# Optimization experiments

Measured on AMD Instinct MI355X. Metric: run time of the kernel, lower is better.

## Reference

```python
import jax, jax.numpy as jnp
import numpy as np

N, E = 50000, 300000
IN_DIM, CODE_DIM = 1024, 768
HID, HEADS, DH = 256, 4, 64
NUM_REL = 5
CODE_WEIGHT = 1.0


def setup_inputs() -> dict:
    key = jax.random.key(0)
    ks = jax.random.split(key, 24)
    p = lambda k, shape: jax.random.normal(k, shape, dtype=jnp.float32) * 0.05
    return {
        "x": jax.random.normal(ks[0], (N, IN_DIM), dtype=jnp.float32),
        "edge_index": jax.random.randint(ks[1], (2, E), 0, N, dtype=jnp.int64),
        "edge_type": jax.random.randint(ks[2], (E,), 0, NUM_REL, dtype=jnp.int64),
        "edge_weight": jax.random.uniform(ks[3], (E,), dtype=jnp.float32),
        "rel_emb": p(ks[4], (NUM_REL, HID)),
        "W_in": p(ks[5], (HID, IN_DIM)),
        "b_in": jnp.zeros((HID,), jnp.float32),
        "W1": p(ks[6], (HEADS * DH, HID)),
        "a1_src": p(ks[7], (HEADS, DH)),
        "a1_dst": p(ks[8], (HEADS, DH)),
        "b1": jnp.zeros((HEADS * DH,), jnp.float32),
        "W2": p(ks[9], (HEADS * DH, HID)),
        "a2_src": p(ks[10], (HEADS, DH)),
        "a2_dst": p(ks[11], (HEADS, DH)),
        "b2": jnp.zeros((HEADS * DH,), jnp.float32),
        "ln1_g": jnp.ones((HID,), jnp.float32),
        "ln1_b": jnp.zeros((HID,), jnp.float32),
        "ln2_g": jnp.ones((HID,), jnp.float32),
        "ln2_b": jnp.zeros((HID,), jnp.float32),
        "W_out": p(ks[12], (1, HID)),
        "b_out": jnp.zeros((1,), jnp.float32),
    }


def _layer_norm(x, g, b, eps=1e-5):
    m = x.mean(-1, keepdims=True)
    v = ((x - m) ** 2).mean(-1, keepdims=True)
    return (x - m) * jax.lax.rsqrt(v + eps) * g + b


def _gat_conv(h, s_all, d_all, W, a_src, a_dst, bias):
    # PyG GATConv (concat=True, negative_slope=0.2), self-loops already in s_all/d_all
    xh = (h @ W.T).reshape(N, HEADS, DH)                      # [N,H,DH]
    al_s = (xh * a_src).sum(-1)                                # [N,H]
    al_d = (xh * a_dst).sum(-1)                                # [N,H]
    e = jax.nn.leaky_relu(al_s[s_all] + al_d[d_all], 0.2)      # [E+N,H]
    mx = jax.ops.segment_max(e, d_all, num_segments=N)         # segment softmax over dst
    ex = jnp.exp(e - mx[d_all])
    den = jax.ops.segment_sum(ex, d_all, num_segments=N)
    alpha = ex / (den[d_all] + 1e-16)
    out = jax.ops.segment_sum(xh[s_all] * alpha[:, :, None], d_all, num_segments=N)
    return out.reshape(N, HEADS * DH) + bias


def reference(x, edge_index, edge_type, edge_weight, rel_emb, W_in, b_in,
              W1, a1_src, a1_dst, b1, W2, a2_src, a2_dst, b2,
              ln1_g, ln1_b, ln2_g, ln2_b, W_out, b_out):
    # split (code_at_front=True), standardize numeric, l2-normalize code
    x_code = x[:, :CODE_DIM]
    x_num = x[:, CODE_DIM:]
    m = x_num.mean(0, keepdims=True)
    s = jnp.maximum(x_num.std(0, ddof=1, keepdims=True), 1e-6)
    x_num = (x_num - m) / s
    nrm = jnp.maximum(jnp.linalg.norm(x_code, axis=1, keepdims=True), 1e-12)
    x_code = x_code / nrm
    xin = jnp.concatenate([x_num, CODE_WEIGHT * x_code], axis=-1)

    h = jax.nn.relu(xin @ W_in.T + b_in)                       # [N,HID]

    src, dst = edge_index[0], edge_index[1]
    rel = rel_emb[edge_type] * edge_weight[:, None]            # [E,HID]
    msg = h[src] + rel
    h = h.at[dst].add(msg)                                     # index_add

    loop = jnp.arange(N, dtype=src.dtype)                      # GATConv add_self_loops
    s_all = jnp.concatenate([src, loop])
    d_all = jnp.concatenate([dst, loop])

    h1 = _gat_conv(h, s_all, d_all, W1, a1_src, a1_dst, b1)
    h = _layer_norm(h1 + h, ln1_g, ln1_b)
    h2 = _gat_conv(h, s_all, d_all, W2, a2_src, a2_dst, b2)
    h = _layer_norm(h2 + h, ln2_g, ln2_b)
    return (h @ W_out.T + b_out).squeeze(-1)                   # [N]
```

## Files before the change

kernel.cpp:

```cpp
#include <hip/hip_runtime.h>
#include <math.h>

constexpr int NN   = 50000;
constexpr int EE   = 300000;
constexpr int IND  = 1024;
constexpr int CODE = 768;
constexpr int HID  = 256;

typedef __bf16 bf16_t;
typedef bf16_t bf16x4 __attribute__((ext_vector_type(4)));
typedef bf16_t bf16x8 __attribute__((ext_vector_type(8)));
typedef float  f32x4  __attribute__((ext_vector_type(4)));

__device__ __forceinline__ f32x4 mfma16(bf16x8 a, bf16x8 b, f32x4 c) {
    return __builtin_amdgcn_mfma_f32_16x16x32_bf16(a, b, c, 0, 0, 0);
}

#define GLOAD_LDS16(gp, lp) __builtin_amdgcn_global_load_lds(                         \
    (__attribute__((address_space(1))) void*)(gp),                                    \
    (__attribute__((address_space(3))) void*)(lp), 16, 0, 0)

__device__ __forceinline__ void cvt_split(f32x4 u0, f32x4 u1, bf16x8& hi, bf16x8& lo) {
    #pragma unroll
    for (int i = 0; i < 4; i++) {
        bf16_t h0 = (bf16_t)u0[i];
        hi[i]     = h0;
        lo[i]     = (bf16_t)(u0[i] - (float)h0);
        bf16_t h1 = (bf16_t)u1[i];
        hi[4 + i] = h1;
        lo[4 + i] = (bf16_t)(u1[i] - (float)h1);
    }
}

__device__ __forceinline__ bf16x8 cvt_hi(f32x4 u0, f32x4 u1) {
    bf16x8 h;
    #pragma unroll
    for (int i = 0; i < 4; i++) {
        h[i]     = (bf16_t)u0[i];
        h[4 + i] = (bf16_t)u1[i];
    }
    return h;
}

__device__ __forceinline__ f32x4 ld_bf4(const bf16_t* p) {
    bf16x4 v = *(const bf16x4*)p;
    f32x4 r;
    r[0] = (float)v[0]; r[1] = (float)v[1]; r[2] = (float)v[2]; r[3] = (float)v[3];
    return r;
}

__global__ void colstats_kernel(const float* __restrict__ x, float* __restrict__ sums) {
    int col = threadIdx.x;
    float s = 0.f, s2 = 0.f;
    for (int row = blockIdx.x; row < NN; row += gridDim.x) {
        float v = x[(size_t)row * IND + CODE + col];
        s += v; s2 += v * v;
    }
    atomicAdd(&sums[col], s);
    atomicAdd(&sums[256 + col], s2);
}

__global__ void rownorm_kernel(const float* __restrict__ x, float* __restrict__ invnorm) {
    int lane = threadIdx.x & 63;
    int wid  = threadIdx.x >> 6;
    int row  = blockIdx.x * 4 + wid;
    if (row >= NN) return;
    const float4* x4 = (const float4*)(x + (size_t)row * IND);
    float s = 0.f;
    #pragma unroll
    for (int i = 0; i < 3; i++) {
        float4 v = x4[lane + i * 64];
        s += v.x * v.x + v.y * v.y + v.z * v.z + v.w * v.w;
    }
    #pragma unroll
    for (int off = 32; off; off >>= 1) s += __shfl_xor(s, off);
    if (lane == 0) invnorm[row] = 1.f / fmaxf(sqrtf(s), 1e-12f);
}

__global__ void prep_w_kernel(const float* __restrict__ W, const float* __restrict__ sums,
                              const float* __restrict__ b_in, bf16_t* __restrict__ Wh,
                              float* __restrict__ cb)
{
    int c = blockIdx.x, t = threadIdx.x;
    float mean = sums[t] / (float)NN;
    float var  = (sums[256 + t] - (float)NN * mean * mean) / (float)(NN - 1);
    float sd   = fmaxf(sqrtf(fmaxf(var, 0.f)), 1e-6f);
    float invstd = 1.f / sd;

    const float* wr = W + (size_t)c * IND;
    bf16_t* wh = Wh + (size_t)c * IND;
    for (int k = t; k < 768; k += 256) wh[k] = (bf16_t)wr[256 + k];
    wh[768 + t] = (bf16_t)(wr[t] * invstd);

    float p = wr[t] * invstd * mean;
    #pragma unroll
    for (int off = 32; off; off >>= 1) p += __shfl_xor(p, off);
    __shared__ float ps[4];
    if ((t & 63) == 0) ps[t >> 6] = p;
    __syncthreads();
    if (t == 0) cb[c] = b_in[c] - (ps[0] + ps[1] + ps[2] + ps[3]);
}

__global__ void prep_ws_kernel(const float* __restrict__ W1, const float* __restrict__ W2,
                               bf16_t* __restrict__ Wh1, bf16_t* __restrict__ Wh2)
{
    int c = blockIdx.x, t = threadIdx.x;
    if (c < 256) Wh1[(size_t)c * 256 + t] = (bf16_t)W1[(size_t)c * 256 + t];
    else {
        int cc = c - 256;
        Wh2[(size_t)cc * 256 + t] = (bf16_t)W2[(size_t)cc * 256 + t];
    }
}


__device__ __forceinline__ void stage_a(const float* __restrict__ src, int ldk,
                                        int rowbase, int maxrow, int k0,
                                        float* ldsbuf, int tid) {
    int w = tid >> 6, l = tid & 63;
    int lr = l >> 3, lc = l & 7;
    int g  = lc ^ lr;
    #pragma unroll
    for (int i = 0; i < 4; i++) {
        int rloc = i * 32 + w * 8;
        float* dst = ldsbuf + rloc * 32;
        int row = rowbase + rloc + lr;
        if (row > maxrow) row = maxrow;
        const float* gp = src + (size_t)row * ldk + k0 + g * 4;
        GLOAD_LDS16(gp, dst);
    }
}

__device__ __forceinline__ void stage_b(const bf16_t* __restrict__ src, int n0, int ldk,
                                        int k0, bf16_t* buf, int tid) {
    int w = tid >> 6, l = tid & 63;
    #pragma unroll
    for (int i = 0; i < 2; i++) {
        int gbase = w * 128 + i * 64;
        bf16_t* dst = buf + gbase * 8;
        int g = gbase + l;
        int col = g >> 2, p = g & 3;
        int gs = p ^ ((col >> 1) & 3);
        const bf16_t* gp = src + (size_t)(n0 + col) * ldk + k0 + gs * 8;
        GLOAD_LDS16(gp, dst);
    }
}

template<int MODE, int K, int FATTN>
__global__ __launch_bounds__(256) void gemm_mfma_kernel(
    const float* __restrict__ A, const bf16_t* __restrict__ Bh,
    const float* __restrict__ cb, const float* __restrict__ invnorm,
    const float* __restrict__ a_src, const float* __restrict__ a_dst,
    float* __restrict__ out, bf16_t* __restrict__ xhb,
    float* __restrict__ al_s, float* __restrict__ al_d)
{
    __shared__ float  As[2][128 * 32];
    __shared__ bf16_t Bhs[2][128 * 32];
    __shared__ float inv_s[128];
    constexpr int NT = K / 32;

    int tid  = threadIdx.x;
    int lane = tid & 63;
    int w    = tid >> 6;
    int wr   = w >> 1, wc = w & 1;
    int r0   = blockIdx.x * 128, n0 = blockIdx.y * 128;

    if (MODE == 1 && tid < 128) {
        int r = r0 + tid;
        inv_s[tid] = (r < NN) ? invnorm[r] : 1.f;
    }

    f32x4 acc[4][4];
    #pragma unroll
    for (int i = 0; i < 4; i++)
        #pragma unroll
        for (int j = 0; j < 4; j++) acc[i][j] = (f32x4)0.f;

    int kc = lane >> 4, fr = lane & 15;

    stage_a(A, K, r0, NN - 1, 0, As[0], tid);
    stage_b(Bh, n0, K, 0, Bhs[0], tid);
    __syncthreads();

    for (int t = 0; t < NT; ++t) {
        int buf = t & 1;
        if (t + 1 < NT) {
            stage_a(A, K, r0, NN - 1, (t + 1) * 32, As[buf ^ 1], tid);
            stage_b(Bh, n0, K, (t + 1) * 32, Bhs[buf ^ 1], tid);
        }
        if (MODE == 1 && t == 24) {
            #pragma unroll
            for (int mf = 0; mf < 4; mf++) {
                f32x4 iv = *(const f32x4*)&inv_s[wr * 64 + mf * 16 + kc * 4];
                #pragma unroll
                for (int nf = 0; nf < 4; nf++)
                    #pragma unroll
                    for (int j = 0; j < 4; j++) acc[mf][nf][j] *= iv[j];
            }
        }
        const float*  Ab = As[buf];
        const bf16_t* Hb = Bhs[buf];
        bf16x8 ahi[4], alo[4];
        #pragma unroll
        for (int mf = 0; mf < 4; mf++) {
            int r  = wr * 64 + mf * 16 + fr;
            int rb = r * 32, r7 = r & 7;
            f32x4 u0 = *(const f32x4*)&Ab[rb + (((2 * kc + 0) ^ r7) << 2)];
            f32x4 u1 = *(const f32x4*)&Ab[rb + (((2 * kc + 1) ^ r7) << 2)];
            if (MODE == 1) cvt_split(u0, u1, ahi[mf], alo[mf]);
            else           ahi[mf] = cvt_hi(u0, u1);
        }
        #pragma unroll
        for (int nf = 0; nf < 4; nf++) {
            int c  = wc * 64 + nf * 16 + fr;
            int pr = kc ^ ((c >> 1) & 3);
            bf16x8 bhi = *(const bf16x8*)&Hb[c * 32 + pr * 8];
            #pragma unroll
            for (int mf = 0; mf < 4; mf++) {
                acc[mf][nf] = mfma16(ahi[mf], bhi, acc[mf][nf]);
                if (MODE == 1) acc[mf][nf] = mfma16(alo[mf], bhi, acc[mf][nf]);
            }
        }
        __syncthreads();
    }

    int head = blockIdx.y * 2 + wc;
    float asv[4], adv[4];
    if (FATTN) {
        #pragma unroll
        for (int nf = 0; nf < 4; nf++) {
            asv[nf] = a_src[head * 64 + nf * 16 + fr];
            adv[nf] = a_dst[head * 64 + nf * 16 + fr];
        }
    }
    #pragma unroll
    for (int mf = 0; mf < 4; mf++) {
        #pragma unroll
        for (int j = 0; j < 4; j++) {
            int row = r0 + wr * 64 + mf * 16 + kc * 4 + j;
            bool ok = row < NN;
            float s = 0.f, d = 0.f;
            #pragma unroll
            for (int nf = 0; nf < 4; nf++) {
                int col = n0 + wc * 64 + nf * 16 + fr;
                float v = acc[mf][nf][j];
                if (MODE == 1) {
                    v = fmaxf(v + cb[col], 0.f);
                    if (ok) out[(size_t)row * HID + col] = v;
                }
                if (FATTN) {
                    s += v * asv[nf]; d += v * adv[nf];
                    if (ok) xhb[(size_t)row * HID + col] = (bf16_t)v;
                }
            }
            if (FATTN) {
                #pragma unroll
                for (int off = 1; off < 16; off <<= 1) {
                    s += __shfl_xor(s, off);
                    d += __shfl_xor(d, off);
                }
                if (ok && fr == 0) {
                    al_s[row * 4 + head] = s;
                    al_d[row * 4 + head] = d;
                }
            }
        }
    }
}

__global__ void deg_kernel(const int* __restrict__ ei, int* __restrict__ deg) {
    int e = blockIdx.x * 256 + threadIdx.x;
    if (e < EE) atomicAdd(&deg[ei[EE + e]], 1);
}

constexpr int SCB = 1024;
constexpr int SCN = (NN + SCB - 1) / SCB;

__global__ void scan_pass1(const int* __restrict__ deg, int* __restrict__ bsum) {
    int b = blockIdx.x, t = threadIdx.x;
    int base = b * SCB + t * 4;
    int s = 0;
    #pragma unroll
    for (int i = 0; i < 4; i++) { int idx = base + i; if (idx < NN) s += deg[idx]; }
    #pragma unroll
    for (int off = 32; off; off >>= 1) s += __shfl_xor(s, off);
    __shared__ int ps[4];
    if ((t & 63) == 0) ps[t >> 6] = s;
    __syncthreads();
    if (t == 0) bsum[b] = ps[0] + ps[1] + ps[2] + ps[3];
}

__global__ void scan_pass2(int* __restrict__ bsum) {
    int t = threadIdx.x;
    int orig = (t < SCN) ? bsum[t] : 0;
    int v = orig;
    for (int off = 1; off < 64; off <<= 1) {
        int u = __shfl_up(v, off);
        if (t >= off) v += u;
    }
    if (t < SCN) bsum[t] = v - orig;
}

__global__ void scan_pass3(const int* __restrict__ deg, const int* __restrict__ boffs,
                           int* __restrict__ row_ptr, int* __restrict__ cursor) {
    int b = blockIdx.x, t = threadIdx.x;
    int base = b * SCB + t * 4;
    int d[4]; int tot = 0;
    #pragma unroll
    for (int i = 0; i < 4; i++) { int idx = base + i; d[i] = (idx < NN) ? deg[idx] : 0; tot += d[i]; }
    int v = tot;
    for (int off = 1; off < 64; off <<= 1) {
        int u = __shfl_up(v, off);
        if ((t & 63) >= off) v += u;
    }
    __shared__ int wsum[4];
    if ((t & 63) == 63) wsum[t >> 6] = v;
    __syncthreads();
    int woff = 0;
    for (int j = 0; j < (t >> 6); j++) woff += wsum[j];
    int run = boffs[b] + woff + v - tot;
    #pragma unroll
    for (int i = 0; i < 4; i++) {
        int idx = base + i;
        if (idx < NN) {
            cursor[idx] = run;
            run += d[i];
            row_ptr[idx + 1] = run;
        }
    }
    if (b == 0 && t == 0) row_ptr[0] = 0;
}

__global__ void fill_kernel(const int* __restrict__ ei, const int* __restrict__ etype,
                            const float* __restrict__ ew, int* __restrict__ cursor,
                            int* __restrict__ csr_src, int* __restrict__ csr_t,
                            float* __restrict__ csr_w) {
    int e = blockIdx.x * 256 + threadIdx.x;
    if (e >= EE) return;
    int dst = ei[EE + e];
    int pos = atomicAdd(&cursor[dst], 1);
    csr_src[pos] = ei[e];
    csr_t[pos]   = etype[e];
    csr_w[pos]   = ew[e];
}

__global__ void relagg_kernel(const float* __restrict__ h, const int* __restrict__ row_ptr,
                              const int* __restrict__ csr_src, const int* __restrict__ csr_t,
                              const float* __restrict__ csr_w,
                              const float* __restrict__ rel_emb, float* __restrict__ out)
{
    int lane = threadIdx.x & 63, wid = threadIdx.x >> 6;
    int node = blockIdx.x * 4 + wid;
    if (node >= NN) return;
    int c0 = lane * 4;
    f32x4 acc = *(const f32x4*)(h + (size_t)node * HID + c0);
    float wsum[5] = {0.f, 0.f, 0.f, 0.f, 0.f};
    int beg = row_ptr[node], end = row_ptr[node + 1];
    int k = beg;
    for (; k + 4 <= end; k += 4) {
        int s[4], tt[4]; float ww[4];
        #pragma unroll
        for (int j = 0; j < 4; j++) {
            s[j]  = csr_src[k + j];
            tt[j] = csr_t[k + j];
            ww[j] = csr_w[k + j];
        }
        f32x4 xv[4];
        #pragma unroll
        for (int j = 0; j < 4; j++) xv[j] = *(const f32x4*)(h + (size_t)s[j] * HID + c0);
        #pragma unroll
        for (int j = 0; j < 4; j++) {
            acc += xv[j];
            #pragma unroll
            for (int r = 0; r < 5; r++) wsum[r] += (tt[j] == r) ? ww[j] : 0.f;
        }
    }
    for (; k < end; k++) {
        int src = csr_src[k]; int t = csr_t[k]; float w = csr_w[k];
        acc += *(const f32x4*)(h + (size_t)src * HID + c0);
        #pragma unroll
        for (int r = 0; r < 5; r++) wsum[r] += (t == r) ? w : 0.f;
    }
    #pragma unroll
    for (int r = 0; r < 5; r++)
        acc += wsum[r] * *(const f32x4*)(rel_emb + r * HID + c0);
    *(f32x4*)(out + (size_t)node * HID + c0) = acc;
}

template<int FINAL>
__global__ void gat_kernel(const bf16_t* __restrict__ xhb, const float* __restrict__ al_s,
                           const float* __restrict__ al_d, const int* __restrict__ row_ptr,
                           const int* __restrict__ csr_src, const float* __restrict__ h_res,
                           const float* __restrict__ bias, const float* __restrict__ ln_g,
                           const float* __restrict__ ln_b, float* __restrict__ out,
                           const float* __restrict__ W_out, const float* __restrict__ b_out,
                           float* __restrict__ final_out)
{
    int lane = threadIdx.x & 63, wid = threadIdx.x >> 6;
    int node = blockIdx.x * 4 + wid;
    if (node >= NN) return;
    int hh = lane >> 4;
    int c0 = lane * 4;

    float ald = al_d[node * 4 + hh];
    float m, den;
    f32x4 acc;

    {
        float als = al_s[node * 4 + hh];
        float e = als + ald;
        e = (e >= 0.f) ? e : 0.2f * e;
        m = e; den = 1.f;
        acc = ld_bf4(xhb + (size_t)node * HID + c0);
    }

    int beg = row_ptr[node], end = row_ptr[node + 1];
    int k = beg;
    for (; k + 4 <= end; k += 4) {
        int s[4];
        #pragma unroll
        for (int j = 0; j < 4; j++) s[j] = csr_src[k + j];
        float als[4];
        #pragma unroll
        for (int j = 0; j < 4; j++) als[j] = al_s[s[j] * 4 + hh];
        f32x4 xv[4];
        #pragma unroll
        for (int j = 0; j < 4; j++) xv[j] = ld_bf4(xhb + (size_t)s[j] * HID + c0);
        #pragma unroll
        for (int j = 0; j < 4; j++) {
            float e = als[j] + ald;
            e = (e >= 0.f) ? e : 0.2f * e;
            float mn  = fmaxf(m, e);
            float f   = __expf(m - mn);
            float wgt = __expf(e - mn);
            m   = mn;
            den = den * f + wgt;
            acc = acc * f + wgt * xv[j];
        }
    }
    for (; k < end; k++) {
        int src = csr_src[k];
        float als = al_s[src * 4 + hh];
        f32x4 xv = ld_bf4(xhb + (size_t)src * HID + c0);
        float e = als + ald;
        e = (e >= 0.f) ? e : 0.2f * e;
        float mn  = fmaxf(m, e);
        float f   = __expf(m - mn);
        float wgt = __expf(e - mn);
        m   = mn;
        den = den * f + wgt;
        acc = acc * f + wgt * xv;
    }

    f32x4 bia = *(const f32x4*)(bias + c0);
    f32x4 res = *(const f32x4*)(h_res + (size_t)node * HID + c0);
    f32x4 z;
    float rd = 1.f / (den + 1e-16f);
    #pragma unroll
    for (int i = 0; i < 4; i++) z[i] = acc[i] * rd + bia[i] + res[i];

    float s = z[0] + z[1] + z[2] + z[3];
    #pragma unroll
    for (int off = 32; off; off >>= 1) s += __shfl_xor(s, off);
    float mean = s * (1.f / 256.f);
    float vp = 0.f;
    #pragma unroll
    for (int i = 0; i < 4; i++) { float d2 = z[i] - mean; vp += d2 * d2; }
    #pragma unroll
    for (int off = 32; off; off >>= 1) vp += __shfl_xor(vp, off);
    float rstd = rsqrtf(vp * (1.f / 256.f) + 1e-5f);

    f32x4 g = *(const f32x4*)(ln_g + c0);
    f32x4 bb = *(const f32x4*)(ln_b + c0);
    if (FINAL) {
        f32x4 wo = *(const f32x4*)(W_out + c0);
        float dot = 0.f;
        #pragma unroll
        for (int i = 0; i < 4; i++)
            dot += ((z[i] - mean) * rstd * g[i] + bb[i]) * wo[i];
        #pragma unroll
        for (int off = 32; off; off >>= 1) dot += __shfl_xor(dot, off);
        if (lane == 0) final_out[node] = dot + b_out[0];
    } else {
        f32x4 o;
        #pragma unroll
        for (int i = 0; i < 4; i++) o[i] = (z[i] - mean) * rstd * g[i] + bb[i];
        *(f32x4*)(out + (size_t)node * HID + c0) = o;
    }
}

extern "C" void kernel_launch(void* const* d_in, const int* in_sizes, int n_in,
                              void* d_out, int out_size, void* d_ws, size_t ws_size,
                              hipStream_t stream) {
    const float* x       = (const float*)d_in[0];
    const int*   ei      = (const int*)d_in[1];
    const int*   etype   = (const int*)d_in[2];
    const float* ew      = (const float*)d_in[3];
    const float* rel_emb = (const float*)d_in[4];
    const float* W_in    = (const float*)d_in[5];
    const float* b_in    = (const float*)d_in[6];
    const float* W1      = (const float*)d_in[7];
    const float* a1s     = (const float*)d_in[8];
    const float* a1d     = (const float*)d_in[9];
    const float* b1      = (const float*)d_in[10];
    const float* W2      = (const float*)d_in[11];
    const float* a2s     = (const float*)d_in[12];
    const float* a2d     = (const float*)d_in[13];
    const float* b2      = (const float*)d_in[14];
    const float* ln1g    = (const float*)d_in[15];
    const float* ln1b    = (const float*)d_in[16];
    const float* ln2g    = (const float*)d_in[17];
    const float* ln2b    = (const float*)d_in[18];
    const float* W_out   = (const float*)d_in[19];
    const float* b_out   = (const float*)d_in[20];
    float* out = (float*)d_out;

    char* ws = (char*)d_ws;
    auto alloc = [&](size_t bytes) {
        void* p = (void*)ws;
        ws += (bytes + 255) & ~(size_t)255;
        return p;
    };
    float*  bufA     = (float*)alloc((size_t)NN * HID * 4);
    float*  bufB     = (float*)alloc((size_t)NN * HID * 4);
    bf16_t* xhb      = (bf16_t*)alloc((size_t)NN * HID * 2);
    bf16_t* wmh      = (bf16_t*)alloc((size_t)HID * IND * 2);
    bf16_t* w1h      = (bf16_t*)alloc((size_t)HID * HID * 2);
    bf16_t* w2h      = (bf16_t*)alloc((size_t)HID * HID * 2);
    float*  cbv      = (float*)alloc(256 * 4);
    float*  stats_s  = (float*)alloc(512 * 4);
    float*  invnorm  = (float*)alloc((size_t)NN * 4);
    float*  al_s     = (float*)alloc((size_t)NN * 4 * 4);
    float*  al_d     = (float*)alloc((size_t)NN * 4 * 4);
    int*    deg      = (int*)alloc((size_t)NN * 4);
    int*    row_ptr  = (int*)alloc((size_t)(NN + 1) * 4);
    int*    cursor   = (int*)alloc((size_t)NN * 4);
    int*    csr_src  = (int*)alloc((size_t)EE * 4);
    int*    csr_t    = (int*)alloc((size_t)EE * 4);
    float*  csr_w    = (float*)alloc((size_t)EE * 4);
    int*    bsum     = (int*)alloc(64 * 4);

    hipMemsetAsync(stats_s, 0, 512 * 4, stream);
    hipMemsetAsync(deg, 0, (size_t)NN * 4, stream);

    colstats_kernel<<<1024, 256, 0, stream>>>(x, stats_s);
    rownorm_kernel<<<(NN + 3) / 4, 256, 0, stream>>>(x, invnorm);
    prep_w_kernel<<<256, 256, 0, stream>>>(W_in, stats_s, b_in, wmh, cbv);
    prep_ws_kernel<<<512, 256, 0, stream>>>(W1, W2, w1h, w2h);

    deg_kernel<<<(EE + 255) / 256, 256, 0, stream>>>(ei, deg);
    scan_pass1<<<SCN, 256, 0, stream>>>(deg, bsum);
    scan_pass2<<<1, 64, 0, stream>>>(bsum);
    scan_pass3<<<SCN, 256, 0, stream>>>(deg, bsum, row_ptr, cursor);
    fill_kernel<<<(EE + 255) / 256, 256, 0, stream>>>(ei, etype, ew, cursor,
                                                      csr_src, csr_t, csr_w);

    dim3 g1((NN + 127) / 128, 2);

    gemm_mfma_kernel<1, 1024, 0><<<g1, 256, 0, stream>>>(
        x, wmh, cbv, invnorm, nullptr, nullptr, bufA, nullptr, nullptr, nullptr);

    int nodeBlocks = (NN + 3) / 4;

    relagg_kernel<<<nodeBlocks, 256, 0, stream>>>(bufA, row_ptr, csr_src, csr_t, csr_w,
                                                  rel_emb, bufB);

    gemm_mfma_kernel<0, 256, 1><<<g1, 256, 0, stream>>>(
        bufB, w1h, nullptr, nullptr, a1s, a1d, nullptr, xhb, al_s, al_d);
    gat_kernel<0><<<nodeBlocks, 256, 0, stream>>>(xhb, al_s, al_d, row_ptr, csr_src,
                                                  bufB, b1, ln1g, ln1b, bufA,
                                                  nullptr, nullptr, nullptr);

    gemm_mfma_kernel<0, 256, 1><<<g1, 256, 0, stream>>>(
        bufA, w2h, nullptr, nullptr, a2s, a2d, nullptr, xhb, al_s, al_d);
    gat_kernel<1><<<nodeBlocks, 256, 0, stream>>>(xhb, al_s, al_d, row_ptr, csr_src,
                                                  bufA, b2, ln2g, ln2b, nullptr,
                                                  W_out, b_out, out);
}
```

Baseline: 423.0 us.

## Feed GAT GEMMs bf16 activations from producers and unroll gathers by eight

```diff
diff --git a/kernel.cpp b/kernel.cpp
--- a/kernel.cpp
+++ b/kernel.cpp
@@ -30,16 +30,6 @@
         hi[4 + i] = h1;
         lo[4 + i] = (bf16_t)(u1[i] - (float)h1);
     }
-}
-
-__device__ __forceinline__ bf16x8 cvt_hi(f32x4 u0, f32x4 u1) {
-    bf16x8 h;
-    #pragma unroll
-    for (int i = 0; i < 4; i++) {
-        h[i]     = (bf16_t)u0[i];
-        h[4 + i] = (bf16_t)u1[i];
-    }
-    return h;
 }
 
 __device__ __forceinline__ f32x4 ld_bf4(const bf16_t* p) {
@@ -131,7 +121,7 @@
 }
 
 __device__ __forceinline__ void stage_b(const bf16_t* __restrict__ src, int n0, int ldk,
-                                        int k0, bf16_t* buf, int tid) {
+                                        int maxrow, int k0, bf16_t* buf, int tid) {
     int w = tid >> 6, l = tid & 63;
     #pragma unroll
     for (int i = 0; i < 2; i++) {
@@ -140,20 +130,25 @@
         int g = gbase + l;
         int col = g >> 2, p = g & 3;
         int gs = p ^ ((col >> 1) & 3);
-        const bf16_t* gp = src + (size_t)(n0 + col) * ldk + k0 + gs * 8;
+        int row = n0 + col;
+        if (row > maxrow) row = maxrow;
+        const bf16_t* gp = src + (size_t)row * ldk + k0 + gs * 8;
         GLOAD_LDS16(gp, dst);
     }
 }
 
 template<int MODE, int K, int FATTN>
 __global__ __launch_bounds__(256) void gemm_mfma_kernel(
-    const float* __restrict__ A, const bf16_t* __restrict__ Bh,
-    const float* __restrict__ cb, const float* __restrict__ invnorm,
-    const float* __restrict__ a_src, const float* __restrict__ a_dst,
-    float* __restrict__ out, bf16_t* __restrict__ xhb,
-    float* __restrict__ al_s, float* __restrict__ al_d)
+    const float* __restrict__ A, const bf16_t* __restrict__ A16,
+    const bf16_t* __restrict__ Bh, const float* __restrict__ cb,
+    const float* __restrict__ invnorm, const float* __restrict__ a_src,
+    const float* __restrict__ a_dst, float* __restrict__ out,
+    bf16_t* __restrict__ xhb, float* __restrict__ al_s, float* __restrict__ al_d)
 {
-    __shared__ float  As[2][128 * 32];
+    constexpr int ASZF = (MODE == 1) ? 2 * 128 * 32 : 8;
+    constexpr int ASZB = (MODE == 0) ? 2 * 128 * 32 : 8;
+    __shared__ float  Asf[ASZF];
+    __shared__ bf16_t Asb[ASZB];
     __shared__ bf16_t Bhs[2][128 * 32];
     __shared__ float inv_s[128];
     constexpr int NT = K / 32;
@@ -177,15 +172,17 @@
 
     int kc = lane >> 4, fr = lane & 15;
 
-    stage_a(A, K, r0, NN - 1, 0, As[0], tid);
-    stage_b(Bh, n0, K, 0, Bhs[0], tid);
+    if (MODE == 1) stage_a(A, K, r0, NN - 1, 0, Asf, tid);
+    else           stage_b(A16, r0, K, NN - 1, 0, Asb, tid);
+    stage_b(Bh, n0, K, 255, 0, Bhs[0], tid);
     __syncthreads();
 
     for (int t = 0; t < NT; ++t) {
         int buf = t & 1;
         if (t + 1 < NT) {
-            stage_a(A, K, r0, NN - 1, (t + 1) * 32, As[buf ^ 1], tid);
-            stage_b(Bh, n0, K, (t + 1) * 32, Bhs[buf ^ 1], tid);
+            if (MODE == 1) stage_a(A, K, r0, NN - 1, (t + 1) * 32, Asf + (buf ^ 1) * (128 * 32), tid);
+            else           stage_b(A16, r0, K, NN - 1, (t + 1) * 32, Asb + (buf ^ 1) * (128 * 32), tid);
+            stage_b(Bh, n0, K, 255, (t + 1) * 32, Bhs[buf ^ 1], tid);
         }
         if (MODE == 1 && t == 24) {
             #pragma unroll
@@ -197,17 +194,22 @@
                     for (int j = 0; j < 4; j++) acc[mf][nf][j] *= iv[j];
             }
         }
-        const float*  Ab = As[buf];
         const bf16_t* Hb = Bhs[buf];
         bf16x8 ahi[4], alo[4];
         #pragma unroll
         for (int mf = 0; mf < 4; mf++) {
-            int r  = wr * 64 + mf * 16 + fr;
-            int rb = r * 32, r7 = r & 7;
-            f32x4 u0 = *(const f32x4*)&Ab[rb + (((2 * kc + 0) ^ r7) << 2)];
-            f32x4 u1 = *(const f32x4*)&Ab[rb + (((2 * kc + 1) ^ r7) << 2)];
-            if (MODE == 1) cvt_split(u0, u1, ahi[mf], alo[mf]);
-            else           ahi[mf] = cvt_hi(u0, u1);
+            int r = wr * 64 + mf * 16 + fr;
+            if (MODE == 1) {
+                const float* Ab = Asf + buf * (128 * 32);
+                int rb = r * 32, r7 = r & 7;
+                f32x4 u0 = *(const f32x4*)&Ab[rb + (((2 * kc + 0) ^ r7) << 2)];
+                f32x4 u1 = *(const f32x4*)&Ab[rb + (((2 * kc + 1) ^ r7) << 2)];
+                cvt_split(u0, u1, ahi[mf], alo[mf]);
+            } else {
+                const bf16_t* Ab = Asb + buf * (128 * 32);
+                int pr = kc ^ ((r >> 1) & 3);
+                ahi[mf] = *(const bf16x8*)&Ab[r * 32 + pr * 8];
+            }
         }
         #pragma unroll
         for (int nf = 0; nf < 4; nf++) {
@@ -346,7 +348,8 @@
 __global__ void relagg_kernel(const float* __restrict__ h, const int* __restrict__ row_ptr,
                               const int* __restrict__ csr_src, const int* __restrict__ csr_t,
                               const float* __restrict__ csr_w,
-                              const float* __restrict__ rel_emb, float* __restrict__ out)
+                              const float* __restrict__ rel_emb, float* __restrict__ out,
+                              bf16_t* __restrict__ out16)
 {
     int lane = threadIdx.x & 63, wid = threadIdx.x >> 6;
     int node = blockIdx.x * 4 + wid;
@@ -355,35 +358,36 @@
     f32x4 acc = *(const f32x4*)(h + (size_t)node * HID + c0);
     float wsum[5] = {0.f, 0.f, 0.f, 0.f, 0.f};
     int beg = row_ptr[node], end = row_ptr[node + 1];
-    int k = beg;
-    for (; k + 4 <= end; k += 4) {
-        int s[4], tt[4]; float ww[4];
-        #pragma unroll
-        for (int j = 0; j < 4; j++) {
-            s[j]  = csr_src[k + j];
-            tt[j] = csr_t[k + j];
-            ww[j] = csr_w[k + j];
-        }
-        f32x4 xv[4];
-        #pragma unroll
-        for (int j = 0; j < 4; j++) xv[j] = *(const f32x4*)(h + (size_t)s[j] * HID + c0);
-        #pragma unroll
-        for (int j = 0; j < 4; j++) {
-            acc += xv[j];
+    for (int k = beg; k < end; k += 8) {
+        int s[8], tt[8]; float ww[8], vm[8];
+        #pragma unroll
+        for (int j = 0; j < 8; j++) {
+            int kk = k + j;
+            bool valid = kk < end;
+            kk = valid ? kk : (end - 1);
+            s[j]  = csr_src[kk];
+            tt[j] = csr_t[kk];
+            ww[j] = valid ? csr_w[kk] : 0.f;
+            vm[j] = valid ? 1.f : 0.f;
+        }
+        f32x4 xv[8];
+        #pragma unroll
+        for (int j = 0; j < 8; j++) xv[j] = *(const f32x4*)(h + (size_t)s[j] * HID + c0);
+        #pragma unroll
+        for (int j = 0; j < 8; j++) {
+            acc += vm[j] * xv[j];
             #pragma unroll
             for (int r = 0; r < 5; r++) wsum[r] += (tt[j] == r) ? ww[j] : 0.f;
         }
-    }
-    for (; k < end; k++) {
-        int src = csr_src[k]; int t = csr_t[k]; float w = csr_w[k];
-        acc += *(const f32x4*)(h + (size_t)src * HID + c0);
-        #pragma unroll
-        for (int r = 0; r < 5; r++) wsum[r] += (t == r) ? w : 0.f;
     }
     #pragma unroll
     for (int r = 0; r < 5; r++)
         acc += wsum[r] * *(const f32x4*)(rel_emb + r * HID + c0);
     *(f32x4*)(out + (size_t)node * HID + c0) = acc;
+    bf16x4 a16;
+    #pragma unroll
+    for (int i = 0; i < 4; i++) a16[i] = (bf16_t)acc[i];
+    *(bf16x4*)(out16 + (size_t)node * HID + c0) = a16;
 }
 
 template<int FINAL>
@@ -392,6 +396,7 @@
                            const int* __restrict__ csr_src, const float* __restrict__ h_res,
                            const float* __restrict__ bias, const float* __restrict__ ln_g,
                            const float* __restrict__ ln_b, float* __restrict__ out,
+                           bf16_t* __restrict__ out16,
                            const float* __restrict__ W_out, const float* __restrict__ b_out,
                            float* __restrict__ final_out)
 {
@@ -414,19 +419,23 @@
     }
 
     int beg = row_ptr[node], end = row_ptr[node + 1];
-    int k = beg;
-    for (; k + 4 <= end; k += 4) {
-        int s[4];
-        #pragma unroll
-        for (int j = 0; j < 4; j++) s[j] = csr_src[k + j];
-        float als[4];
-        #pragma unroll
-        for (int j = 0; j < 4; j++) als[j] = al_s[s[j] * 4 + hh];
-        f32x4 xv[4];
-        #pragma unroll
-        for (int j = 0; j < 4; j++) xv[j] = ld_bf4(xhb + (size_t)s[j] * HID + c0);
-        #pragma unroll
-        for (int j = 0; j < 4; j++) {
+    for (int k = beg; k < end; k += 8) {
+        int s[8]; float als[8];
+        #pragma unroll
+        for (int j = 0; j < 8; j++) {
+            int kk = k + j;
+            bool valid = kk < end;
+            s[j] = csr_src[valid ? kk : (end - 1)];
+            als[j] = valid ? 0.f : -INFINITY;
+        }
+        #pragma unroll
+        for (int j = 0; j < 8; j++)
+            if (als[j] == 0.f) als[j] = al_s[s[j] * 4 + hh];
+        f32x4 xv[8];
+        #pragma unroll
+        for (int j = 0; j < 8; j++) xv[j] = ld_bf4(xhb + (size_t)s[j] * HID + c0);
+        #pragma unroll
+        for (int j = 0; j < 8; j++) {
             float e = als[j] + ald;
             e = (e >= 0.f) ? e : 0.2f * e;
             float mn  = fmaxf(m, e);
@@ -437,19 +446,6 @@
             acc = acc * f + wgt * xv[j];
         }
     }
-    for (; k < end; k++) {
-        int src = csr_src[k];
-        float als = al_s[src * 4 + hh];
-        f32x4 xv = ld_bf4(xhb + (size_t)src * HID + c0);
-        float e = als + ald;
-        e = (e >= 0.f) ? e : 0.2f * e;
-        float mn  = fmaxf(m, e);
-        float f   = __expf(m - mn);
-        float wgt = __expf(e - mn);
-        m   = mn;
-        den = den * f + wgt;
-        acc = acc * f + wgt * xv;
-    }
 
     f32x4 bia = *(const f32x4*)(bias + c0);
     f32x4 res = *(const f32x4*)(h_res + (size_t)node * HID + c0);
@@ -482,9 +478,14 @@
         if (lane == 0) final_out[node] = dot + b_out[0];
     } else {
         f32x4 o;
-        #pragma unroll
-        for (int i = 0; i < 4; i++) o[i] = (z[i] - mean) * rstd * g[i] + bb[i];
+        bf16x4 o16;
+        #pragma unroll
+        for (int i = 0; i < 4; i++) {
+            o[i] = (z[i] - mean) * rstd * g[i] + bb[i];
+            o16[i] = (bf16_t)o[i];
+        }
         *(f32x4*)(out + (size_t)node * HID + c0) = o;
+        *(bf16x4*)(out16 + (size_t)node * HID + c0) = o16;
     }
 }
 
@@ -523,6 +524,7 @@
     float*  bufA     = (float*)alloc((size_t)NN * HID * 4);
     float*  bufB     = (float*)alloc((size_t)NN * HID * 4);
     bf16_t* xhb      = (bf16_t*)alloc((size_t)NN * HID * 2);
+    bf16_t* gin16    = (bf16_t*)alloc((size_t)NN * HID * 2);
     bf16_t* wmh      = (bf16_t*)alloc((size_t)HID * IND * 2);
     bf16_t* w1h      = (bf16_t*)alloc((size_t)HID * HID * 2);
     bf16_t* w2h      = (bf16_t*)alloc((size_t)HID * HID * 2);
@@ -557,22 +559,22 @@
     dim3 g1((NN + 127) / 128, 2);
 
     gemm_mfma_kernel<1, 1024, 0><<<g1, 256, 0, stream>>>(
-        x, wmh, cbv, invnorm, nullptr, nullptr, bufA, nullptr, nullptr, nullptr);
+        x, nullptr, wmh, cbv, invnorm, nullptr, nullptr, bufA, nullptr, nullptr, nullptr);
 
     int nodeBlocks = (NN + 3) / 4;
 
     relagg_kernel<<<nodeBlocks, 256, 0, stream>>>(bufA, row_ptr, csr_src, csr_t, csr_w,
-                                                  rel_emb, bufB);
+                                                  rel_emb, bufB, gin16);
 
     gemm_mfma_kernel<0, 256, 1><<<g1, 256, 0, stream>>>(
-        bufB, w1h, nullptr, nullptr, a1s, a1d, nullptr, xhb, al_s, al_d);
+        nullptr, gin16, w1h, nullptr, nullptr, a1s, a1d, nullptr, xhb, al_s, al_d);
     gat_kernel<0><<<nodeBlocks, 256, 0, stream>>>(xhb, al_s, al_d, row_ptr, csr_src,
-                                                  bufB, b1, ln1g, ln1b, bufA,
+                                                  bufB, b1, ln1g, ln1b, bufA, gin16,
                                                   nullptr, nullptr, nullptr);
 
     gemm_mfma_kernel<0, 256, 1><<<g1, 256, 0, stream>>>(
-        bufA, w2h, nullptr, nullptr, a2s, a2d, nullptr, xhb, al_s, al_d);
+        nullptr, gin16, w2h, nullptr, nullptr, a2s, a2d, nullptr, xhb, al_s, al_d);
     gat_kernel<1><<<nodeBlocks, 256, 0, stream>>>(xhb, al_s, al_d, row_ptr, csr_src,
-                                                  bufA, b2, ln2g, ln2b, nullptr,
+                                                  bufA, b2, ln2g, ln2b, nullptr, nullptr,
                                                   W_out, b_out, out);
 }
```

New measurement: 427.7 us. About the same (+1.1%).
